# Performance work log

Measured on AMD Instinct MI355X. Metric: run time of the kernel, lower is better.

Reference implementation:

```python
import jax, jax.numpy as jnp
import numpy as np

N = 100_000   # nodes
E = 3_200_000 # edges (avg degree 32)

def _glorot(k, shape):
    fan_in, fan_out = shape
    lim = float(np.sqrt(6.0 / (fan_in + fan_out)))
    return jax.random.uniform(k, shape, jnp.float32, -lim, lim)

def setup_inputs() -> dict:
    key = jax.random.key(0)
    ks = jax.random.split(key, 8)
    x = jax.random.normal(ks[0], (N, 3), dtype=jnp.float32)
    edge_index = jax.random.randint(ks[1], (2, E), 0, N, dtype=jnp.int32)
    choices = jax.random.bernoulli(ks[2], 0.5, (N,))
    W1 = _glorot(ks[3], (3, 16));  b1 = jnp.zeros((16,), jnp.float32)
    W2 = _glorot(ks[4], (16, 16)); b2 = jnp.zeros((16,), jnp.float32)
    W3 = _glorot(ks[5], (16, 1));  b3 = jnp.zeros((1,), jnp.float32)
    fc_w = _glorot(ks[6], (16, 1)); fc_b = jnp.zeros((1,), jnp.float32)
    return dict(x=x, edge_index=edge_index, choices=choices,
                W1=W1, b1=b1, W2=W2, b2=b2, W3=W3, b3=b3,
                fc_w=fc_w, fc_b=fc_b)

def reference(x, edge_index, choices, W1, b1, W2, b2, W3, b3, fc_w, fc_b):
    row, col = edge_index[0], edge_index[1]  # source -> target
    # improved=True GCN norm: self-loop weight 2, deg = in_degree + 2
    deg = jax.ops.segment_sum(jnp.ones((E,), x.dtype), col, num_segments=N) + 2.0
    dinv = jax.lax.rsqrt(deg)                    # [N]
    enorm = dinv[row] * dinv[col]                # [E] edge normalization
    self_norm = 2.0 * dinv * dinv                # [N] self-loop term

    def gcn(h, W, b):
        h = h @ W                                # [N, F_out]
        agg = jax.ops.segment_sum(h[row] * enorm[:, None], col, num_segments=N)
        return agg + self_norm[:, None] * h + b

    h = jax.nn.relu(gcn(x, W1, b1))
    h = jax.nn.relu(gcn(h, W2, b2))
    c = gcn(h, W3, b3)[:, 0]                     # [N] per-node logit
    # masked softmax over chosen nodes (torch masked_select + softmax,
    # expressed with static shape: non-chosen entries get probability 0)
    logits = jnp.where(choices, c, -jnp.inf)
    choice = jax.nn.softmax(logits, axis=0)      # [N]
    # global_mean_pool with a single graph = mean over all nodes
    v = jnp.mean(h, axis=0, keepdims=True)       # [1, 16]
    value = v @ fc_w + fc_b                      # [1, 1]
    return choice, value
```

## Files before the change

### kernel.cpp

```cpp
#include <hip/hip_runtime.h>
#include <hip/hip_fp16.h>
#include <math.h>

#define BLK 256


#define BSH 8
#define NB 512
#define CAP 10240
#define EB 8192
#define BINTH 512

__device__ inline float4 load_h4(const __half* base, int node, int sub) {
    const uint2* p = reinterpret_cast<const uint2*>(base + ((size_t)node << 4)) + sub;
    uint2 u = *p;
    union { unsigned u; __half2 h; } a, b;
    a.u = u.x; b.u = u.y;
    float2 fa = __half22float2(a.h), fb = __half22float2(b.h);
    return make_float4(fa.x, fa.y, fb.x, fb.y);
}

__device__ inline void store_h4(__half* base, int node, int sub, float4 v) {
    union { unsigned u; __half2 h; } a, b;
    a.h = __floats2half2_rn(v.x, v.y);
    b.h = __floats2half2_rn(v.z, v.w);
    uint2 u; u.x = a.u; u.y = b.u;
    *(reinterpret_cast<uint2*>(base + ((size_t)node << 4)) + sub) = u;
}

__device__ inline float3 load_xs(const __half* xs, int node) {
    uint2 u = *reinterpret_cast<const uint2*>(xs + ((size_t)node << 2));
    union { unsigned u; __half2 h; } a, b;
    a.u = u.x; b.u = u.y;
    float2 fa = __half22float2(a.h), fb = __half22float2(b.h);
    return make_float3(fa.x, fa.y, fb.x);
}

__device__ inline unsigned encf(float f) {
    unsigned u = __float_as_uint(f);
    return (u & 0x80000000u) ? ~u : (u | 0x80000000u);
}
__device__ inline float decf(unsigned e) {
    return (e & 0x80000000u) ? __uint_as_float(e ^ 0x80000000u)
                             : __uint_as_float(~e);
}

__global__ void k_init(int* __restrict__ gcur, float* __restrict__ scal) {
    int t = threadIdx.x;
    gcur[t] = 0;
    if (t < 18) scal[t] = 0.f;
}

__global__ void __launch_bounds__(BINTH) k_bin(const int* __restrict__ row,
                                               const int* __restrict__ col,
                                               int* __restrict__ gcur,
                                               int* __restrict__ packed, int E) {
    __shared__ int stage[EB];
    __shared__ unsigned short sbuk[EB];
    __shared__ int hist[NB];
    __shared__ int lscan[NB];
    __shared__ int cur[NB];
    __shared__ int gbase[NB];
    int tid = threadIdx.x;
    int base = blockIdx.x * EB;
    int cnt = min(EB, E - base);

    hist[tid] = 0;
    __syncthreads();
    for (int j = tid; j < cnt; j += BINTH) {
        int c = __builtin_nontemporal_load(col + base + j);
        atomicAdd(&hist[c >> BSH], 1);
    }
    __syncthreads();
    lscan[tid] = hist[tid];
    __syncthreads();
    for (int d = 1; d < NB; d <<= 1) {
        int t = (tid >= d) ? lscan[tid - d] : 0;
        __syncthreads();
        if (tid >= d) lscan[tid] += t;
        __syncthreads();
    }
    {
        int ex = lscan[tid] - hist[tid];
        lscan[tid] = ex;
        cur[tid] = ex;
    }
    __syncthreads();
    for (int j = tid; j < cnt; j += BINTH) {
        int c = __builtin_nontemporal_load(col + base + j);
        int r = __builtin_nontemporal_load(row + base + j);
        int b = c >> BSH;
        int p = atomicAdd(&cur[b], 1);
        stage[p] = (r << BSH) | (c & ((1 << BSH) - 1));
        sbuk[p] = (unsigned short)b;
    }
    __syncthreads();
    if (hist[tid] > 0) gbase[tid] = tid * CAP + atomicAdd(&gcur[tid], hist[tid]);
    __syncthreads();
    for (int j = tid; j < cnt; j += BINTH) {
        int b = sbuk[j];
        int pos = gbase[b] + (j - lscan[b]);
        packed[pos] = stage[j];
    }
}

__global__ void __launch_bounds__(BLK) k_place(const int* __restrict__ packed,
                                               const int* __restrict__ bcnt,
                                               const float* __restrict__ x,
                                               int* __restrict__ degi,
                                               int* __restrict__ offs,
                                               float* __restrict__ dinv,
                                               __half* __restrict__ xs,
                                               int* __restrict__ srcs, int n) {
    __shared__ int cnt[256];
    __shared__ int lcur[256];
    __shared__ int ssum[256];
    __shared__ int psum[256];
    int tid = threadIdx.x;
    int b = blockIdx.x;
    int pv = 0;
    for (int t = tid; t < b; t += BLK) pv += bcnt[t];
    psum[tid] = pv;
    cnt[tid] = 0;
    __syncthreads();
    for (int d = BLK / 2; d > 0; d >>= 1) {
        if (tid < d) psum[tid] += psum[tid + d];
        __syncthreads();
    }
    int pbeg = psum[0];
    int ecnt = bcnt[b];
    const int* pk = packed + (size_t)b * CAP;
    for (int j = tid; j < ecnt; j += BLK)
        atomicAdd(&cnt[pk[j] & 255], 1);
    __syncthreads();
    int c = cnt[tid];
    ssum[tid] = c;
    __syncthreads();
    for (int d = 1; d < 256; d <<= 1) {
        int t = (tid >= d) ? ssum[tid - d] : 0;
        __syncthreads();
        if (tid >= d) ssum[tid] += t;
        __syncthreads();
    }
    int ex = ssum[tid] - c;
    lcur[tid] = ex;
    int i = (b << BSH) + tid;
    if (i < n) {
        degi[i] = c;
        offs[i] = pbeg + ex;
        float di = rsqrtf((float)c + 2.0f);
        dinv[i] = di;
        float x0 = x[i * 3 + 0], x1 = x[i * 3 + 1], x2 = x[i * 3 + 2];
        union { unsigned u; __half2 h; } a2, b2;
        a2.h = __floats2half2_rn(di * x0, di * x1);
        b2.h = __floats2half2_rn(di * x2, 0.f);
        uint2 u; u.x = a2.u; u.y = b2.u;
        *reinterpret_cast<uint2*>(xs + ((size_t)i << 2)) = u;
    }
    __syncthreads();
    for (int j = tid; j < ecnt; j += BLK) {
        int v = pk[j];
        int li = v & 255;
        int slot = atomicAdd(&lcur[li], 1);
        srcs[pbeg + slot] = v >> BSH;
    }
}

__global__ void __launch_bounds__(BLK) k_agg1(const __half* __restrict__ xs,
                                              const int* __restrict__ offs,
                                              const int* __restrict__ degi,
                                              const int* __restrict__ srcs,
                                              const float* __restrict__ dinv,
                                              const float* __restrict__ b1,
                                              const float* __restrict__ W1,
                                              const float* __restrict__ W2,
                                              __half* __restrict__ hwsB, int n) {
    __shared__ float w1[48];
    __shared__ float w2[256];
    __shared__ float bb[16];
    __shared__ float hbuf[64][17];
    int tid = threadIdx.x;
    w2[tid] = W2[tid];
    if (tid < 48) w1[tid] = W1[tid];
    if (tid < 16) bb[tid] = b1[tid];
    __syncthreads();
    int nl = tid >> 2, sub = tid & 3;
    int i = blockIdx.x * 64 + nl;
    bool act = (i < n);
    float di = 0.f;
    if (act) {
        di = dinv[i];
        float ax = 0.f, ay = 0.f, az = 0.f;
        float bx = 0.f, by = 0.f, bz = 0.f;
        int beg = offs[i], end = beg + degi[i];
        int j = beg + sub;
        for (; j + 12 < end; j += 16) {
            int r0 = srcs[j], r1 = srcs[j + 4], r2 = srcs[j + 8], r3 = srcs[j + 12];
            float3 q0 = load_xs(xs, r0);
            float3 q1 = load_xs(xs, r1);
            float3 q2 = load_xs(xs, r2);
            float3 q3 = load_xs(xs, r3);
            ax += q0.x; ay += q0.y; az += q0.z;
            bx += q1.x; by += q1.y; bz += q1.z;
            ax += q2.x; ay += q2.y; az += q2.z;
            bx += q3.x; by += q3.y; bz += q3.z;
        }
        for (; j < end; j += 4) {
            float3 q0 = load_xs(xs, srcs[j]);
            ax += q0.x; ay += q0.y; az += q0.z;
        }
        ax += bx; ay += by; az += bz;
        ax += __shfl_xor(ax, 1); ay += __shfl_xor(ay, 1); az += __shfl_xor(az, 1);
        ax += __shfl_xor(ax, 2); ay += __shfl_xor(ay, 2); az += __shfl_xor(az, 2);
        float3 s = load_xs(xs, i);
        ax += 2.f * s.x; ay += 2.f * s.y; az += 2.f * s.z;
#pragma unroll
        for (int k = 0; k < 4; k++) {
            int f = sub * 4 + k;
            float hv = di * (ax * w1[f] + ay * w1[16 + f] + az * w1[32 + f]) + bb[f];
            hbuf[nl][f] = fmaxf(hv, 0.f);
        }
    }
    __syncthreads();
    if (act) {
        const float* hn = hbuf[nl];
        float s0 = 0.f, s1 = 0.f, s2 = 0.f, s3 = 0.f;
#pragma unroll
        for (int f = 0; f < 16; f++) {
            float hv = hn[f];
            const float4 wq = *(const float4*)&w2[f * 16 + sub * 4];
            s0 += hv * wq.x; s1 += hv * wq.y; s2 += hv * wq.z; s3 += hv * wq.w;
        }
        store_h4(hwsB, i, sub, make_float4(di * s0, di * s1, di * s2, di * s3));
    }
}

#define GATHER8H(HWS)                                                           \
    float4 acc;                                                                 \
    {                                                                           \
        float4 s0 = load_h4(HWS, i, sub);                                       \
        acc = make_float4(2.f * s0.x, 2.f * s0.y, 2.f * s0.z, 2.f * s0.w);      \
        float4 a1 = make_float4(0.f, 0.f, 0.f, 0.f);                            \
        float4 a2 = a1, a3 = a1;                                                \
        int beg = offs[i], end = beg + degi[i];                                 \
        int j = beg;                                                            \
        for (; j + 7 < end; j += 8) {                                           \
            int r0 = srcs[j],     r1 = srcs[j + 1], r2 = srcs[j + 2], r3 = srcs[j + 3]; \
            int r4 = srcs[j + 4], r5 = srcs[j + 5], r6 = srcs[j + 6], r7 = srcs[j + 7]; \
            float4 q0 = load_h4(HWS, r0, sub);                                  \
            float4 q1 = load_h4(HWS, r1, sub);                                  \
            float4 q2 = load_h4(HWS, r2, sub);                                  \
            float4 q3 = load_h4(HWS, r3, sub);                                  \
            float4 q4 = load_h4(HWS, r4, sub);                                  \
            float4 q5 = load_h4(HWS, r5, sub);                                  \
            float4 q6 = load_h4(HWS, r6, sub);                                  \
            float4 q7 = load_h4(HWS, r7, sub);                                  \
            acc.x += q0.x + q4.x; acc.y += q0.y + q4.y;                         \
            acc.z += q0.z + q4.z; acc.w += q0.w + q4.w;                         \
            a1.x += q1.x + q5.x; a1.y += q1.y + q5.y;                           \
            a1.z += q1.z + q5.z; a1.w += q1.w + q5.w;                           \
            a2.x += q2.x + q6.x; a2.y += q2.y + q6.y;                           \
            a2.z += q2.z + q6.z; a2.w += q2.w + q6.w;                           \
            a3.x += q3.x + q7.x; a3.y += q3.y + q7.y;                           \
            a3.z += q3.z + q7.z; a3.w += q3.w + q7.w;                           \
        }                                                                       \
        for (; j < end; j++) {                                                  \
            float4 q0 = load_h4(HWS, srcs[j], sub);                             \
            acc.x += q0.x; acc.y += q0.y; acc.z += q0.z; acc.w += q0.w;         \
        }                                                                       \
        acc.x += a1.x + a2.x + a3.x;                                            \
        acc.y += a1.y + a2.y + a3.y;                                            \
        acc.z += a1.z + a2.z + a3.z;                                            \
        acc.w += a1.w + a2.w + a3.w;                                            \
    }

__global__ void __launch_bounds__(BLK) k_agg2(const __half* __restrict__ hwsB,
                                              const int* __restrict__ offs,
                                              const int* __restrict__ degi,
                                              const int* __restrict__ srcs,
                                              const float* __restrict__ dinv,
                                              const float* __restrict__ b2,
                                              const float* __restrict__ W3,
                                              float* __restrict__ hws3,
                                              float* __restrict__ pool, int n) {
    __shared__ float w3[16];
    __shared__ float bb[16];
    __shared__ float lp[16];
    int tid = threadIdx.x;
    if (tid < 16) { w3[tid] = W3[tid]; bb[tid] = b2[tid]; lp[tid] = 0.f; }
    __syncthreads();
    int nl = tid >> 2, sub = tid & 3;
    int i = blockIdx.x * 64 + nl;
    bool act = (i < n);
    float4 h = make_float4(0.f, 0.f, 0.f, 0.f);
    if (act) {
        float di = dinv[i];
        GATHER8H(hwsB);
        h.x = fmaxf(di * acc.x + bb[sub * 4 + 0], 0.f);
        h.y = fmaxf(di * acc.y + bb[sub * 4 + 1], 0.f);
        h.z = fmaxf(di * acc.z + bb[sub * 4 + 2], 0.f);
        h.w = fmaxf(di * acc.w + bb[sub * 4 + 3], 0.f);
        float p = h.x * w3[sub * 4 + 0] + h.y * w3[sub * 4 + 1]
                + h.z * w3[sub * 4 + 2] + h.w * w3[sub * 4 + 3];
        p += __shfl_xor(p, 1);
        p += __shfl_xor(p, 2);
        if (sub == 0) hws3[i] = di * p;
    }
    float4 hp = h;
#pragma unroll
    for (int m = 4; m < 64; m <<= 1) {
        hp.x += __shfl_xor(hp.x, m);
        hp.y += __shfl_xor(hp.y, m);
        hp.z += __shfl_xor(hp.z, m);
        hp.w += __shfl_xor(hp.w, m);
    }
    if ((tid & 63) < 4) {
        atomicAdd(&lp[sub * 4 + 0], hp.x);
        atomicAdd(&lp[sub * 4 + 1], hp.y);
        atomicAdd(&lp[sub * 4 + 2], hp.z);
        atomicAdd(&lp[sub * 4 + 3], hp.w);
    }
    __syncthreads();
    if (tid < 16) atomicAdd(&pool[tid], lp[tid]);
}

__global__ void __launch_bounds__(BLK) k_agg3(const float* __restrict__ hws3,
                                              const int* __restrict__ offs,
                                              const int* __restrict__ degi,
                                              const int* __restrict__ srcs,
                                              const float* __restrict__ dinv,
                                              const float* __restrict__ b3,
                                              const int* __restrict__ choices,
                                              float* __restrict__ cbuf,
                                              unsigned* __restrict__ menc, int n) {
    __shared__ float red[BLK];
    int tid = threadIdx.x;
    int nl = tid >> 2, sub = tid & 3;
    int i = blockIdx.x * 64 + nl;
    bool act = (i < n);
    float s = 0.f;
    if (act) {
        int beg = offs[i], end = beg + degi[i];
        int j = beg + sub;
        float s1 = 0.f;
        for (; j + 4 < end; j += 8) {
            float q0 = hws3[srcs[j]];
            float q1 = hws3[srcs[j + 4]];
            s += q0; s1 += q1;
        }
        if (j < end) s += hws3[srcs[j]];
        s += s1;
    }
    s += __shfl_xor(s, 1);
    s += __shfl_xor(s, 2);
    float logit = -INFINITY;
    if (act && sub == 0) {
        float c = dinv[i] * (s + 2.f * hws3[i]) + b3[0];
        cbuf[i] = c;
        if (choices[i] != 0) logit = c;
    }
    red[tid] = logit;
    __syncthreads();
    for (int d = BLK / 2; d > 0; d >>= 1) {
        if (tid < d) red[tid] = fmaxf(red[tid], red[tid + d]);
        __syncthreads();
    }
    if (tid == 0) atomicMax(menc, encf(red[0]));
}

__global__ void __launch_bounds__(BLK) k_sumexp(const float* __restrict__ cbuf,
                                                const int* __restrict__ choices,
                                                const unsigned* __restrict__ menc,
                                                float* __restrict__ Ssum, int n) {
    __shared__ float red[BLK];
    int i = blockIdx.x * BLK + threadIdx.x;
    float m = decf(*menc);
    float v = 0.0f;
    if (i < n && choices[i] != 0) v = expf(cbuf[i] - m);
    red[threadIdx.x] = v;
    __syncthreads();
    for (int d = BLK / 2; d > 0; d >>= 1) {
        if (threadIdx.x < d) red[threadIdx.x] += red[threadIdx.x + d];
        __syncthreads();
    }
    if (threadIdx.x == 0) atomicAdd(Ssum, red[0]);
}

__global__ void __launch_bounds__(BLK) k_final(const float* __restrict__ cbuf,
                                               const int* __restrict__ choices,
                                               const unsigned* __restrict__ menc,
                                               const float* __restrict__ Ssum,
                                               const float* __restrict__ pool,
                                               const float* __restrict__ fcw,
                                               const float* __restrict__ fcb,
                                               float* __restrict__ out, int n) {
    int i = blockIdx.x * BLK + threadIdx.x;
    if (i < n) {
        float p = 0.0f;
        if (choices[i] != 0) {
            float m = decf(*menc), S = Ssum[0];
            p = expf(cbuf[i] - m) / S;
        }
        out[i] = p;
    }
    if (blockIdx.x == 0 && threadIdx.x == 0) {
        float invn = 1.0f / (float)n;
        float v = 0.0f;
#pragma unroll
        for (int f = 0; f < 16; f++) v += (pool[f] * invn) * fcw[f];
        out[n] = v + fcb[0];
    }
}

extern "C" void kernel_launch(void* const* d_in, const int* in_sizes, int n_in,
                              void* d_out, int out_size, void* d_ws, size_t ws_size,
                              hipStream_t stream) {
    const float* x       = (const float*)d_in[0];
    const int*   ei      = (const int*)d_in[1];
    const int*   choices = (const int*)d_in[2];
    const float* W1 = (const float*)d_in[3];
    const float* b1 = (const float*)d_in[4];
    const float* W2 = (const float*)d_in[5];
    const float* b2 = (const float*)d_in[6];
    const float* W3 = (const float*)d_in[7];
    const float* b3 = (const float*)d_in[8];
    const float* fcw = (const float*)d_in[9];
    const float* fcb = (const float*)d_in[10];
    float* out = (float*)d_out;

    int n = in_sizes[0] / 3;
    int E = in_sizes[1] / 2;
    const int* row = ei;
    const int* col = ei + E;

    int nblkN = (n + BLK - 1) / BLK;
    int nblk64 = (n + 63) / 64;
    int nbuck = (n + (1 << BSH) - 1) >> BSH;
    int nblkBin = (E + EB - 1) / EB;

    char* ws = (char*)d_ws;
    size_t o = 0;
    auto alloc = [&](size_t bytes) { char* p = ws + o; o += (bytes + 15) & ~(size_t)15; return p; };
    int*   degi   = (int*)  alloc((size_t)n * 4);
    int*   offs   = (int*)  alloc((size_t)n * 4);
    float* dinv   = (float*)alloc((size_t)n * 4);
    float* hws3   = (float*)alloc((size_t)n * 4);
    float* cbuf   = (float*)alloc((size_t)n * 4);
    int*   gcur   = (int*)  alloc(NB * 4);
    float* scal   = (float*)alloc(256);
    float* Ssum   = scal + 0;
    float* pool   = scal + 1;
    unsigned* menc = (unsigned*)(scal + 17);
    __half* xs    = (__half*)alloc((size_t)n * 4 * 2);
    size_t hw_bytes = (size_t)n * 16 * 2;
    size_t pk_bytes = (size_t)NB * CAP * 4;
    char*  blob   = alloc(hw_bytes > pk_bytes ? hw_bytes : pk_bytes);
    int*    packed = (int*)blob;
    __half* hwsB   = (__half*)blob;
    int*   srcs   = (int*)  alloc((size_t)E * 4);
    (void)ws_size;

    k_init<<<1, NB, 0, stream>>>(gcur, scal);
    k_bin<<<nblkBin, BINTH, 0, stream>>>(row, col, gcur, packed, E);
    k_place<<<nbuck, BLK, 0, stream>>>(packed, gcur, x, degi, offs, dinv, xs, srcs, n);

    k_agg1<<<nblk64, BLK, 0, stream>>>(xs, offs, degi, srcs, dinv, b1, W1, W2, hwsB, n);
    k_agg2<<<nblk64, BLK, 0, stream>>>(hwsB, offs, degi, srcs, dinv, b2, W3, hws3, pool, n);
    k_agg3<<<nblk64, BLK, 0, stream>>>(hws3, offs, degi, srcs, dinv, b3, choices, cbuf, menc, n);

    k_sumexp<<<nblkN, BLK, 0, stream>>>(cbuf, choices, menc, Ssum, n);
    k_final<<<nblkN, BLK, 0, stream>>>(cbuf, choices, menc, Ssum, pool, fcw, fcb, out, n);
}
```

Before: 249.2 us.

## Sort nodes by in-degree within each bucket to balance aggregation wavefronts

```diff
diff --git a/kernel.cpp b/kernel.cpp
--- a/kernel.cpp
+++ b/kernel.cpp
@@ -10,6 +10,7 @@
 #define CAP 10240
 #define EB 8192
 #define BINTH 512
+#define DCLIP 72
 
 __device__ inline float4 load_h4(const __half* base, int node, int sub) {
     const uint2* p = reinterpret_cast<const uint2*>(base + ((size_t)node << 4)) + sub;
@@ -111,17 +112,22 @@
                                                int* __restrict__ offs,
                                                float* __restrict__ dinv,
                                                __half* __restrict__ xs,
-                                               int* __restrict__ srcs, int n) {
+                                               int* __restrict__ srcs,
+                                               int* __restrict__ perm, int n) {
     __shared__ int cnt[256];
     __shared__ int lcur[256];
     __shared__ int ssum[256];
     __shared__ int psum[256];
+    __shared__ int dh[DCLIP];
+    __shared__ int dbase[DCLIP];
     int tid = threadIdx.x;
     int b = blockIdx.x;
+    int nb0 = b << BSH;
     int pv = 0;
     for (int t = tid; t < b; t += BLK) pv += bcnt[t];
     psum[tid] = pv;
     cnt[tid] = 0;
+    if (tid < DCLIP) dh[tid] = 0;
     __syncthreads();
     for (int d = BLK / 2; d > 0; d >>= 1) {
         if (tid < d) psum[tid] += psum[tid + d];
@@ -144,8 +150,10 @@
     }
     int ex = ssum[tid] - c;
     lcur[tid] = ex;
-    int i = (b << BSH) + tid;
-    if (i < n) {
+    int valid = min(n - nb0, 256);
+    int i = nb0 + tid;
+    int dc = (c > DCLIP - 1) ? DCLIP - 1 : c;
+    if (tid < valid) {
         degi[i] = c;
         offs[i] = pbeg + ex;
         float di = rsqrtf((float)c + 2.0f);
@@ -156,6 +164,20 @@
         b2.h = __floats2half2_rn(di * x2, 0.f);
         uint2 u; u.x = a2.u; u.y = b2.u;
         *reinterpret_cast<uint2*>(xs + ((size_t)i << 2)) = u;
+        atomicAdd(&dh[dc], 1);
+    }
+    __syncthreads();
+    if (tid == 0) {
+        int run = 0;
+#pragma unroll 1
+        for (int d = 0; d < DCLIP; d++) { dbase[d] = run; run += dh[d]; dh[d] = 0; }
+    }
+    __syncthreads();
+    if (tid < valid) {
+        int r = atomicAdd(&dh[dc], 1);
+        perm[(b << 8) + dbase[dc] + r] = i;
+    } else {
+        perm[(b << 8) + tid] = -1;
     }
     __syncthreads();
     for (int j = tid; j < ecnt; j += BLK) {
@@ -171,6 +193,7 @@
                                               const int* __restrict__ degi,
                                               const int* __restrict__ srcs,
                                               const float* __restrict__ dinv,
+                                              const int* __restrict__ perm,
                                               const float* __restrict__ b1,
                                               const float* __restrict__ W1,
                                               const float* __restrict__ W2,
@@ -185,8 +208,8 @@
     if (tid < 16) bb[tid] = b1[tid];
     __syncthreads();
     int nl = tid >> 2, sub = tid & 3;
-    int i = blockIdx.x * 64 + nl;
-    bool act = (i < n);
+    int i = perm[blockIdx.x * 64 + nl];
+    bool act = (i >= 0);
     float di = 0.f;
     if (act) {
         di = dinv[i];
@@ -279,6 +302,7 @@
                                               const int* __restrict__ degi,
                                               const int* __restrict__ srcs,
                                               const float* __restrict__ dinv,
+                                              const int* __restrict__ perm,
                                               const float* __restrict__ b2,
                                               const float* __restrict__ W3,
                                               float* __restrict__ hws3,
@@ -290,8 +314,8 @@
     if (tid < 16) { w3[tid] = W3[tid]; bb[tid] = b2[tid]; lp[tid] = 0.f; }
     __syncthreads();
     int nl = tid >> 2, sub = tid & 3;
-    int i = blockIdx.x * 64 + nl;
-    bool act = (i < n);
+    int i = perm[blockIdx.x * 64 + nl];
+    bool act = (i >= 0);
     float4 h = make_float4(0.f, 0.f, 0.f, 0.f);
     if (act) {
         float di = dinv[i];
@@ -329,6 +353,7 @@
                                               const int* __restrict__ degi,
                                               const int* __restrict__ srcs,
                                               const float* __restrict__ dinv,
+                                              const int* __restrict__ perm,
                                               const float* __restrict__ b3,
                                               const int* __restrict__ choices,
                                               float* __restrict__ cbuf,
@@ -336,8 +361,8 @@
     __shared__ float red[BLK];
     int tid = threadIdx.x;
     int nl = tid >> 2, sub = tid & 3;
-    int i = blockIdx.x * 64 + nl;
-    bool act = (i < n);
+    int i = perm[blockIdx.x * 64 + nl];
+    bool act = (i >= 0);
     float s = 0.f;
     if (act) {
         int beg = offs[i], end = beg + degi[i];
@@ -434,8 +459,8 @@
     const int* col = ei + E;
 
     int nblkN = (n + BLK - 1) / BLK;
-    int nblk64 = (n + 63) / 64;
     int nbuck = (n + (1 << BSH) - 1) >> BSH;
+    int nblkP = nbuck * 4;
     int nblkBin = (E + EB - 1) / EB;
 
     char* ws = (char*)d_ws;
@@ -446,6 +471,7 @@
     float* dinv   = (float*)alloc((size_t)n * 4);
     float* hws3   = (float*)alloc((size_t)n * 4);
     float* cbuf   = (float*)alloc((size_t)n * 4);
+    int*   perm   = (int*)  alloc((size_t)nbuck * 256 * 4);
     int*   gcur   = (int*)  alloc(NB * 4);
     float* scal   = (float*)alloc(256);
     float* Ssum   = scal + 0;
@@ -462,11 +488,11 @@
 
     k_init<<<1, NB, 0, stream>>>(gcur, scal);
     k_bin<<<nblkBin, BINTH, 0, stream>>>(row, col, gcur, packed, E);
-    k_place<<<nbuck, BLK, 0, stream>>>(packed, gcur, x, degi, offs, dinv, xs, srcs, n);
-
-    k_agg1<<<nblk64, BLK, 0, stream>>>(xs, offs, degi, srcs, dinv, b1, W1, W2, hwsB, n);
-    k_agg2<<<nblk64, BLK, 0, stream>>>(hwsB, offs, degi, srcs, dinv, b2, W3, hws3, pool, n);
-    k_agg3<<<nblk64, BLK, 0, stream>>>(hws3, offs, degi, srcs, dinv, b3, choices, cbuf, menc, n);
+    k_place<<<nbuck, BLK, 0, stream>>>(packed, gcur, x, degi, offs, dinv, xs, srcs, perm, n);
+
+    k_agg1<<<nblkP, BLK, 0, stream>>>(xs, offs, degi, srcs, dinv, perm, b1, W1, W2, hwsB, n);
+    k_agg2<<<nblkP, BLK, 0, stream>>>(hwsB, offs, degi, srcs, dinv, perm, b2, W3, hws3, pool, n);
+    k_agg3<<<nblkP, BLK, 0, stream>>>(hws3, offs, degi, srcs, dinv, perm, b3, choices, cbuf, menc, n);
 
     k_sumexp<<<nblkN, BLK, 0, stream>>>(cbuf, choices, menc, Ssum, n);
     k_final<<<nblkN, BLK, 0, stream>>>(cbuf, choices, menc, Ssum, pool, fcw, fcb, out, n);
```

New measurement: 262.7 us. 1.05x slower.

## Pad CSR rows to multiples of four and fuse softmax reduction into agg3

Applied to the files above, without the earlier changes.

```diff
diff --git a/kernel.cpp b/kernel.cpp
--- a/kernel.cpp
+++ b/kernel.cpp
@@ -8,6 +8,7 @@
 #define BSH 8
 #define NB 512
 #define CAP 10240
+#define SCAP 11264
 #define EB 8192
 #define BINTH 512
 
@@ -34,15 +35,6 @@
     a.u = u.x; b.u = u.y;
     float2 fa = __half22float2(a.h), fb = __half22float2(b.h);
     return make_float3(fa.x, fa.y, fb.x);
-}
-
-__device__ inline unsigned encf(float f) {
-    unsigned u = __float_as_uint(f);
-    return (u & 0x80000000u) ? ~u : (u | 0x80000000u);
-}
-__device__ inline float decf(unsigned e) {
-    return (e & 0x80000000u) ? __uint_as_float(e ^ 0x80000000u)
-                             : __uint_as_float(~e);
 }
 
 __global__ void k_init(int* __restrict__ gcur, float* __restrict__ scal) {
@@ -115,26 +107,19 @@
     __shared__ int cnt[256];
     __shared__ int lcur[256];
     __shared__ int ssum[256];
-    __shared__ int psum[256];
     int tid = threadIdx.x;
     int b = blockIdx.x;
-    int pv = 0;
-    for (int t = tid; t < b; t += BLK) pv += bcnt[t];
-    psum[tid] = pv;
+    int nb0 = b << BSH;
     cnt[tid] = 0;
     __syncthreads();
-    for (int d = BLK / 2; d > 0; d >>= 1) {
-        if (tid < d) psum[tid] += psum[tid + d];
-        __syncthreads();
-    }
-    int pbeg = psum[0];
     int ecnt = bcnt[b];
     const int* pk = packed + (size_t)b * CAP;
     for (int j = tid; j < ecnt; j += BLK)
         atomicAdd(&cnt[pk[j] & 255], 1);
     __syncthreads();
     int c = cnt[tid];
-    ssum[tid] = c;
+    int pl = (c + 3) & ~3;
+    ssum[tid] = pl;
     __syncthreads();
     for (int d = 1; d < 256; d <<= 1) {
         int t = (tid >= d) ? ssum[tid - d] : 0;
@@ -142,12 +127,13 @@
         if (tid >= d) ssum[tid] += t;
         __syncthreads();
     }
-    int ex = ssum[tid] - c;
-    lcur[tid] = ex;
-    int i = (b << BSH) + tid;
-    if (i < n) {
-        degi[i] = c;
-        offs[i] = pbeg + ex;
+    int A = b * SCAP + (ssum[tid] - pl);
+    lcur[tid] = A;
+    int valid = min(n - nb0, 256);
+    int i = nb0 + tid;
+    if (tid < valid) {
+        degi[i] = pl;
+        offs[i] = A;
         float di = rsqrtf((float)c + 2.0f);
         dinv[i] = di;
         float x0 = x[i * 3 + 0], x1 = x[i * 3 + 1], x2 = x[i * 3 + 2];
@@ -156,13 +142,18 @@
         b2.h = __floats2half2_rn(di * x2, 0.f);
         uint2 u; u.x = a2.u; u.y = b2.u;
         *reinterpret_cast<uint2*>(xs + ((size_t)i << 2)) = u;
+        for (int k = c; k < pl; k++) srcs[A + k] = n;
+    }
+    if (b == 0 && tid == 0) {
+        uint2 z; z.x = 0u; z.y = 0u;
+        *reinterpret_cast<uint2*>(xs + ((size_t)n << 2)) = z;
     }
     __syncthreads();
     for (int j = tid; j < ecnt; j += BLK) {
         int v = pk[j];
         int li = v & 255;
         int slot = atomicAdd(&lcur[li], 1);
-        srcs[pbeg + slot] = v >> BSH;
+        srcs[slot] = v >> BSH;
     }
 }
 
@@ -183,6 +174,8 @@
     w2[tid] = W2[tid];
     if (tid < 48) w1[tid] = W1[tid];
     if (tid < 16) bb[tid] = b1[tid];
+    if (blockIdx.x == 0 && tid < 8)
+        reinterpret_cast<unsigned*>(hwsB + ((size_t)n << 4))[tid] = 0u;
     __syncthreads();
     int nl = tid >> 2, sub = tid & 3;
     int i = blockIdx.x * 64 + nl;
@@ -192,22 +185,15 @@
         di = dinv[i];
         float ax = 0.f, ay = 0.f, az = 0.f;
         float bx = 0.f, by = 0.f, bz = 0.f;
-        int beg = offs[i], end = beg + degi[i];
-        int j = beg + sub;
-        for (; j + 12 < end; j += 16) {
-            int r0 = srcs[j], r1 = srcs[j + 4], r2 = srcs[j + 8], r3 = srcs[j + 12];
-            float3 q0 = load_xs(xs, r0);
-            float3 q1 = load_xs(xs, r1);
-            float3 q2 = load_xs(xs, r2);
-            float3 q3 = load_xs(xs, r3);
-            ax += q0.x; ay += q0.y; az += q0.z;
-            bx += q1.x; by += q1.y; bz += q1.z;
-            ax += q2.x; ay += q2.y; az += q2.z;
-            bx += q3.x; by += q3.y; bz += q3.z;
-        }
-        for (; j < end; j += 4) {
-            float3 q0 = load_xs(xs, srcs[j]);
-            ax += q0.x; ay += q0.y; az += q0.z;
+        int A = offs[i], pc = degi[i];
+        for (int j = A + 4 * sub; j < A + pc; j += 16) {
+            int4 s = *reinterpret_cast<const int4*>(srcs + j);
+            float3 q0 = load_xs(xs, s.x);
+            float3 q1 = load_xs(xs, s.y);
+            float3 q2 = load_xs(xs, s.z);
+            float3 q3 = load_xs(xs, s.w);
+            ax += q0.x + q1.x; ay += q0.y + q1.y; az += q0.z + q1.z;
+            bx += q2.x + q3.x; by += q2.y + q3.y; bz += q2.z + q3.z;
         }
         ax += bx; ay += by; az += bz;
         ax += __shfl_xor(ax, 1); ay += __shfl_xor(ay, 1); az += __shfl_xor(az, 1);
@@ -235,26 +221,26 @@
     }
 }
 
-#define GATHER8H(HWS)                                                           \
+#define GATHERV(HWS)                                                            \
     float4 acc;                                                                 \
     {                                                                           \
         float4 s0 = load_h4(HWS, i, sub);                                       \
         acc = make_float4(2.f * s0.x, 2.f * s0.y, 2.f * s0.z, 2.f * s0.w);      \
         float4 a1 = make_float4(0.f, 0.f, 0.f, 0.f);                            \
         float4 a2 = a1, a3 = a1;                                                \
-        int beg = offs[i], end = beg + degi[i];                                 \
-        int j = beg;                                                            \
-        for (; j + 7 < end; j += 8) {                                           \
-            int r0 = srcs[j],     r1 = srcs[j + 1], r2 = srcs[j + 2], r3 = srcs[j + 3]; \
-            int r4 = srcs[j + 4], r5 = srcs[j + 5], r6 = srcs[j + 6], r7 = srcs[j + 7]; \
-            float4 q0 = load_h4(HWS, r0, sub);                                  \
-            float4 q1 = load_h4(HWS, r1, sub);                                  \
-            float4 q2 = load_h4(HWS, r2, sub);                                  \
-            float4 q3 = load_h4(HWS, r3, sub);                                  \
-            float4 q4 = load_h4(HWS, r4, sub);                                  \
-            float4 q5 = load_h4(HWS, r5, sub);                                  \
-            float4 q6 = load_h4(HWS, r6, sub);                                  \
-            float4 q7 = load_h4(HWS, r7, sub);                                  \
+        int A = offs[i], pc = degi[i];                                          \
+        int j = A;                                                              \
+        for (; j + 8 <= A + pc; j += 8) {                                       \
+            int4 sa = *reinterpret_cast<const int4*>(srcs + j);                 \
+            int4 sb = *reinterpret_cast<const int4*>(srcs + j + 4);             \
+            float4 q0 = load_h4(HWS, sa.x, sub);                                \
+            float4 q1 = load_h4(HWS, sa.y, sub);                                \
+            float4 q2 = load_h4(HWS, sa.z, sub);                                \
+            float4 q3 = load_h4(HWS, sa.w, sub);                                \
+            float4 q4 = load_h4(HWS, sb.x, sub);                                \
+            float4 q5 = load_h4(HWS, sb.y, sub);                                \
+            float4 q6 = load_h4(HWS, sb.z, sub);                                \
+            float4 q7 = load_h4(HWS, sb.w, sub);                                \
             acc.x += q0.x + q4.x; acc.y += q0.y + q4.y;                         \
             acc.z += q0.z + q4.z; acc.w += q0.w + q4.w;                         \
             a1.x += q1.x + q5.x; a1.y += q1.y + q5.y;                           \
@@ -264,9 +250,16 @@
             a3.x += q3.x + q7.x; a3.y += q3.y + q7.y;                           \
             a3.z += q3.z + q7.z; a3.w += q3.w + q7.w;                           \
         }                                                                       \
-        for (; j < end; j++) {                                                  \
-            float4 q0 = load_h4(HWS, srcs[j], sub);                             \
+        if (j < A + pc) {                   \
+            int4 sa = *reinterpret_cast<const int4*>(srcs + j);                 \
+            float4 q0 = load_h4(HWS, sa.x, sub);                                \
+            float4 q1 = load_h4(HWS, sa.y, sub);                                \
+            float4 q2 = load_h4(HWS, sa.z, sub);                                \
+            float4 q3 = load_h4(HWS, sa.w, sub);                                \
             acc.x += q0.x; acc.y += q0.y; acc.z += q0.z; acc.w += q0.w;         \
+            a1.x += q1.x; a1.y += q1.y; a1.z += q1.z; a1.w += q1.w;             \
+            a2.x += q2.x; a2.y += q2.y; a2.z += q2.z; a2.w += q2.w;             \
+            a3.x += q3.x; a3.y += q3.y; a3.z += q3.z; a3.w += q3.w;             \
         }                                                                       \
         acc.x += a1.x + a2.x + a3.x;                                            \
         acc.y += a1.y + a2.y + a3.y;                                            \
@@ -288,6 +281,7 @@
     __shared__ float lp[16];
     int tid = threadIdx.x;
     if (tid < 16) { w3[tid] = W3[tid]; bb[tid] = b2[tid]; lp[tid] = 0.f; }
+    if (blockIdx.x == 0 && tid == 0) hws3[n] = 0.f;
     __syncthreads();
     int nl = tid >> 2, sub = tid & 3;
     int i = blockIdx.x * 64 + nl;
@@ -295,7 +289,7 @@
     float4 h = make_float4(0.f, 0.f, 0.f, 0.f);
     if (act) {
         float di = dinv[i];
-        GATHER8H(hwsB);
+        GATHERV(hwsB);
         h.x = fmaxf(di * acc.x + bb[sub * 4 + 0], 0.f);
         h.y = fmaxf(di * acc.y + bb[sub * 4 + 1], 0.f);
         h.z = fmaxf(di * acc.z + bb[sub * 4 + 2], 0.f);
@@ -332,25 +326,23 @@
                                               const float* __restrict__ b3,
                                               const int* __restrict__ choices,
                                               float* __restrict__ cbuf,
-                                              unsigned* __restrict__ menc, int n) {
+                                              float* __restrict__ bmax,
+                                              float* __restrict__ bsum, int n) {
     __shared__ float red[BLK];
     int tid = threadIdx.x;
     int nl = tid >> 2, sub = tid & 3;
     int i = blockIdx.x * 64 + nl;
     bool act = (i < n);
-    float s = 0.f;
+    float s0 = 0.f, s1 = 0.f;
     if (act) {
-        int beg = offs[i], end = beg + degi[i];
-        int j = beg + sub;
-        float s1 = 0.f;
-        for (; j + 4 < end; j += 8) {
-            float q0 = hws3[srcs[j]];
-            float q1 = hws3[srcs[j + 4]];
-            s += q0; s1 += q1;
+        int A = offs[i], pc = degi[i];
+        for (int j = A + 4 * sub; j < A + pc; j += 16) {
+            int4 s = *reinterpret_cast<const int4*>(srcs + j);
+            s0 += hws3[s.x] + hws3[s.z];
+            s1 += hws3[s.y] + hws3[s.w];
         }
-        if (j < end) s += hws3[srcs[j]];
-        s += s1;
-    }
+    }
+    float s = s0 + s1;
     s += __shfl_xor(s, 1);
     s += __shfl_xor(s, 2);
     float logit = -INFINITY;
@@ -365,30 +357,50 @@
         if (tid < d) red[tid] = fmaxf(red[tid], red[tid + d]);
         __syncthreads();
     }
-    if (tid == 0) atomicMax(menc, encf(red[0]));
-}
-
-__global__ void __launch_bounds__(BLK) k_sumexp(const float* __restrict__ cbuf,
-                                                const int* __restrict__ choices,
-                                                const unsigned* __restrict__ menc,
-                                                float* __restrict__ Ssum, int n) {
+    float bm = red[0];
+    __syncthreads();
+    red[tid] = (logit > -INFINITY) ? expf(logit - bm) : 0.f;
+    __syncthreads();
+    for (int d = BLK / 2; d > 0; d >>= 1) {
+        if (tid < d) red[tid] += red[tid + d];
+        __syncthreads();
+    }
+    if (tid == 0) { bmax[blockIdx.x] = bm; bsum[blockIdx.x] = red[0]; }
+}
+
+__global__ void __launch_bounds__(BLK) k_comb(const float* __restrict__ bmax,
+                                              const float* __restrict__ bsum,
+                                              float* __restrict__ scal_m,
+                                              float* __restrict__ Ssum, int nblk) {
     __shared__ float red[BLK];
-    int i = blockIdx.x * BLK + threadIdx.x;
-    float m = decf(*menc);
-    float v = 0.0f;
-    if (i < n && choices[i] != 0) v = expf(cbuf[i] - m);
-    red[threadIdx.x] = v;
+    int tid = threadIdx.x;
+    float m = -INFINITY;
+    for (int i = tid; i < nblk; i += BLK) m = fmaxf(m, bmax[i]);
+    red[tid] = m;
     __syncthreads();
     for (int d = BLK / 2; d > 0; d >>= 1) {
-        if (threadIdx.x < d) red[threadIdx.x] += red[threadIdx.x + d];
-        __syncthreads();
-    }
-    if (threadIdx.x == 0) atomicAdd(Ssum, red[0]);
+        if (tid < d) red[tid] = fmaxf(red[tid], red[tid + d]);
+        __syncthreads();
+    }
+    float M = red[0];
+    __syncthreads();
+    float s = 0.f;
+    for (int i = tid; i < nblk; i += BLK) {
+        float bm = bmax[i];
+        if (bm > -INFINITY) s += bsum[i] * expf(bm - M);
+    }
+    red[tid] = s;
+    __syncthreads();
+    for (int d = BLK / 2; d > 0; d >>= 1) {
+        if (tid < d) red[tid] += red[tid + d];
+        __syncthreads();
+    }
+    if (tid == 0) { scal_m[0] = M; Ssum[0] = red[0]; }
 }
 
 __global__ void __launch_bounds__(BLK) k_final(const float* __restrict__ cbuf,
                                                const int* __restrict__ choices,
-                                               const unsigned* __restrict__ menc,
+                                               const float* __restrict__ scal_m,
                                                const float* __restrict__ Ssum,
                                                const float* __restrict__ pool,
                                                const float* __restrict__ fcw,
@@ -398,7 +410,7 @@
     if (i < n) {
         float p = 0.0f;
         if (choices[i] != 0) {
-            float m = decf(*menc), S = Ssum[0];
+            float m = scal_m[0], S = Ssum[0];
             p = expf(cbuf[i] - m) / S;
         }
         out[i] = p;
@@ -444,20 +456,22 @@
     int*   degi   = (int*)  alloc((size_t)n * 4);
     int*   offs   = (int*)  alloc((size_t)n * 4);
     float* dinv   = (float*)alloc((size_t)n * 4);
-    float* hws3   = (float*)alloc((size_t)n * 4);
+    float* hws3   = (float*)alloc((size_t)(n + 1) * 4);
     float* cbuf   = (float*)alloc((size_t)n * 4);
+    float* bmax   = (float*)alloc(8192);
+    float* bsum   = (float*)alloc(8192);
     int*   gcur   = (int*)  alloc(NB * 4);
     float* scal   = (float*)alloc(256);
     float* Ssum   = scal + 0;
     float* pool   = scal + 1;
-    unsigned* menc = (unsigned*)(scal + 17);
-    __half* xs    = (__half*)alloc((size_t)n * 4 * 2);
-    size_t hw_bytes = (size_t)n * 16 * 2;
+    float* scal_m = scal + 17;
+    __half* xs    = (__half*)alloc((size_t)(n + 1) * 4 * 2);
+    size_t hw_bytes = (size_t)(n + 1) * 16 * 2;
     size_t pk_bytes = (size_t)NB * CAP * 4;
     char*  blob   = alloc(hw_bytes > pk_bytes ? hw_bytes : pk_bytes);
     int*    packed = (int*)blob;
     __half* hwsB   = (__half*)blob;
-    int*   srcs   = (int*)  alloc((size_t)E * 4);
+    int*   srcs   = (int*)  alloc((size_t)NB * SCAP * 4);
     (void)ws_size;
 
     k_init<<<1, NB, 0, stream>>>(gcur, scal);
@@ -466,8 +480,8 @@
 
     k_agg1<<<nblk64, BLK, 0, stream>>>(xs, offs, degi, srcs, dinv, b1, W1, W2, hwsB, n);
     k_agg2<<<nblk64, BLK, 0, stream>>>(hwsB, offs, degi, srcs, dinv, b2, W3, hws3, pool, n);
-    k_agg3<<<nblk64, BLK, 0, stream>>>(hws3, offs, degi, srcs, dinv, b3, choices, cbuf, menc, n);
-
-    k_sumexp<<<nblkN, BLK, 0, stream>>>(cbuf, choices, menc, Ssum, n);
-    k_final<<<nblkN, BLK, 0, stream>>>(cbuf, choices, menc, Ssum, pool, fcw, fcb, out, n);
-}
+    k_agg3<<<nblk64, BLK, 0, stream>>>(hws3, offs, degi, srcs, dinv, b3, choices, cbuf, bmax, bsum, n);
+
+    k_comb<<<1, BLK, 0, stream>>>(bmax, bsum, scal_m, Ssum, nblk64);
+    k_final<<<nblkN, BLK, 0, stream>>>(cbuf, choices, scal_m, Ssum, pool, fcw, fcb, out, n);
+}
```

Measured after the change: 232.8 us. 6.6% less time.
